# Performance work log

Measured on AMD Instinct MI355X. Metric: run time of the kernel, lower is better.

## Reference

```python
import jax, jax.numpy as jnp
import numpy as np

NUM_HEADS = 8
D_MODEL = 256
DIM = D_MODEL // NUM_HEADS  # 32
EPS = 1e-6


def _proj(x, W, b):
    # Conv1d with kernel_size=1 == channel-mixing matmul over length axis
    return jnp.einsum('oi,bil->bol', W, x) + b[None, :, None]


def _linear_attention(q, k, v):
    # q,k,v: [B, dim, heads, L]
    q = jax.nn.elu(q) + 1.0
    k = jax.nn.elu(k) + 1.0
    L = v.shape[3]
    v = v / L
    # KV: [B, dim_v, dim_k, heads]
    KV = jnp.einsum('bdhm,bqhm->bqdh', k, v)
    # Z: [B, heads, L]
    Z = 1.0 / (jnp.einsum('bdhm,bdh->bhm', q, k.sum(3)) + EPS)
    # out: [B, dim, heads, L]
    return jnp.einsum('bdhm,bqdh,bhm->bqhm', q, KV, Z) * L


def setup_inputs() -> dict:
    key = jax.random.key(0)
    ks = jax.random.split(key, 11)
    B, L = 8, 4096
    s = 0.05
    return {
        'query': jax.random.normal(ks[0], (B, D_MODEL, L), dtype=jnp.float32),
        'key':   jax.random.normal(ks[1], (B, D_MODEL, L), dtype=jnp.float32),
        'value': jax.random.normal(ks[2], (B, D_MODEL, L), dtype=jnp.float32),
        'Wq': jax.random.normal(ks[3], (D_MODEL, D_MODEL), dtype=jnp.float32) * s,
        'bq': jnp.zeros((D_MODEL,), dtype=jnp.float32),
        'Wk': jax.random.normal(ks[4], (D_MODEL, D_MODEL), dtype=jnp.float32) * s,
        'bk': jnp.zeros((D_MODEL,), dtype=jnp.float32),
        'Wv': jax.random.normal(ks[5], (D_MODEL, D_MODEL), dtype=jnp.float32) * s,
        'bv': jnp.zeros((D_MODEL,), dtype=jnp.float32),
        'Wm': jax.random.normal(ks[6], (D_MODEL, D_MODEL), dtype=jnp.float32) * s,
        'bm': jnp.zeros((D_MODEL,), dtype=jnp.float32),
    }


def reference(query, key, value, Wq, bq, Wk, bk, Wv, bv, Wm, bm):
    B = query.shape[0]
    q = _proj(query, Wq, bq).reshape(B, DIM, NUM_HEADS, -1)
    k = _proj(key,   Wk, bk).reshape(B, DIM, NUM_HEADS, -1)
    v = _proj(value, Wv, bv).reshape(B, DIM, NUM_HEADS, -1)
    x = _linear_attention(q, k, v)           # [B, dim, heads, L]
    x = x.reshape(B, D_MODEL, -1)            # merge heads back to channels
    return jnp.einsum('oi,bil->bol', Wm, x) + bm[None, :, None]
```

## Files before the change

kernel.cpp:

```cpp
#include <hip/hip_runtime.h>
#include <math.h>

#define D_MODEL 256
#define NHEADS 8
#define HDIM 32
#define BATCH 8
#define SEQL 4096
#define EPS 1e-6f

typedef _Float16 f16;
typedef _Float16 f16x4 __attribute__((ext_vector_type(4)));
typedef _Float16 f16x8 __attribute__((ext_vector_type(8)));
typedef float f32x4 __attribute__((ext_vector_type(4)));

__device__ __forceinline__ float elu1(float x) {
    return x > 0.f ? x + 1.f : __expf(x);
}

__global__ void prep_kernel(const float* __restrict__ Wq, const float* __restrict__ Wk,
                            const float* __restrict__ Wv, const float* __restrict__ Wm,
                            const float* __restrict__ bq, const float* __restrict__ bk,
                            const float* __restrict__ bv,
                            f16* __restrict__ w16, float* __restrict__ bperm,
                            float* __restrict__ KVz) {
    const int bid = blockIdx.x;
    if (bid < 1024) {
        int idx = bid * 256 + threadIdx.x;
        int mat = idx >> 16, r = (idx >> 8) & 255, c = idx & 255;
        const float* W = (mat == 0) ? Wq : (mat == 1) ? Wk : (mat == 2) ? Wv : Wm;
        float v;
        if (mat < 3) v = W[(size_t)(((r & 31) << 3) + (r >> 5)) * 256 + c];
        else         v = W[(size_t)r * 256 + (((c & 31) << 3) + (c >> 5))];
        w16[idx] = (f16)v;
    } else if (bid == 1024) {
        int t = threadIdx.x;
        bperm[0 * 256 + t] = bq[((t & 31) << 3) + (t >> 5)];
        bperm[1 * 256 + t] = bk[((t & 31) << 3) + (t >> 5)];
        bperm[2 * 256 + t] = bv[((t & 31) << 3) + (t >> 5)];
    } else {
        int i = (bid - 1025) * 256 + threadIdx.x;
        KVz[i] = 0.f;
    }
}

#define BSTR 40
__global__ __launch_bounds__(256, 3) void gemm_stage1(
    const float* __restrict__ Xq, const float* __restrict__ Xk, const float* __restrict__ Xv,
    const f16* __restrict__ w16, const float* __restrict__ bperm,
    f16* __restrict__ yq, f16* __restrict__ yk, f16* __restrict__ yv) {
    __shared__ __align__(16) char smem[18432];
    f16* Bs = (f16*)smem;
    f16* Cb = (f16*)smem;

    const int z = blockIdx.z;
    const int which = z >> 3;
    const int b = z & 7;
    const float* X = (which == 0) ? Xq : (which == 1) ? Xk : Xv;
    const f16* W = w16 + which * 65536;
    f16* Y = (which == 0) ? yq : (which == 1) ? yk : yv;
    const float* bp = bperm + which * 256;

    const int l0 = blockIdx.x * 128;
    const int m0 = blockIdx.y * 128;
    const int tid = threadIdx.x;
    const int wave = tid >> 6, lane = tid & 63;
    const int wm = wave >> 1, wn = wave & 1;
    const int ln = lane & 15, quad = lane >> 4;
    const int bp8 = tid & 7;
    const int bg = tid >> 3;

    const float* Xbase = X + ((size_t)b * D_MODEL + 4 * bp8) * SEQL + l0 + 4 * bg;
    const f16* Wb[4];
#pragma unroll
    for (int mf = 0; mf < 4; ++mf)
        Wb[mf] = W + (size_t)(m0 + wm * 64 + mf * 16 + ln) * 256 + quad * 8;

    float4 xr[4];
    f16x8 afc[4], afn[4];

#define LOADX(K0) do { \
        const float* xb_ = Xbase + (size_t)(K0) * SEQL; \
        xr[0] = *(const float4*)(xb_ + 0 * SEQL); \
        xr[1] = *(const float4*)(xb_ + 1 * SEQL); \
        xr[2] = *(const float4*)(xb_ + 2 * SEQL); \
        xr[3] = *(const float4*)(xb_ + 3 * SEQL); \
    } while (0)

#define STOREB() do { \
        f16x4 w_; \
        w_[0] = (f16)xr[0].x; w_[1] = (f16)xr[1].x; w_[2] = (f16)xr[2].x; w_[3] = (f16)xr[3].x; \
        *(f16x4*)&Bs[(4 * bg + 0) * BSTR + 4 * bp8] = w_; \
        w_[0] = (f16)xr[0].y; w_[1] = (f16)xr[1].y; w_[2] = (f16)xr[2].y; w_[3] = (f16)xr[3].y; \
        *(f16x4*)&Bs[(4 * bg + 1) * BSTR + 4 * bp8] = w_; \
        w_[0] = (f16)xr[0].z; w_[1] = (f16)xr[1].z; w_[2] = (f16)xr[2].z; w_[3] = (f16)xr[3].z; \
        *(f16x4*)&Bs[(4 * bg + 2) * BSTR + 4 * bp8] = w_; \
        w_[0] = (f16)xr[0].w; w_[1] = (f16)xr[1].w; w_[2] = (f16)xr[2].w; w_[3] = (f16)xr[3].w; \
        *(f16x4*)&Bs[(4 * bg + 3) * BSTR + 4 * bp8] = w_; \
    } while (0)

    f32x4 acc[4][4];
#pragma unroll
    for (int mf = 0; mf < 4; ++mf)
#pragma unroll
        for (int nf = 0; nf < 4; ++nf)
#pragma unroll
            for (int r = 0; r < 4; ++r) acc[mf][nf][r] = 0.f;

    LOADX(0);
#pragma unroll
    for (int mf = 0; mf < 4; ++mf) afc[mf] = *(const f16x8*)(Wb[mf] + 0);

#pragma unroll
    for (int it = 0; it < 8; ++it) {
        const int k0 = it * 32;
        __syncthreads();
        STOREB();
        __syncthreads();
        if (it < 7) {
            LOADX(k0 + 32);
#pragma unroll
            for (int mf = 0; mf < 4; ++mf)
                afn[mf] = *(const f16x8*)(Wb[mf] + k0 + 32);
        }
        f16x8 bf[4];
#pragma unroll
        for (int nf = 0; nf < 4; ++nf)
            bf[nf] = *(const f16x8*)&Bs[(wn * 64 + nf * 16 + ln) * BSTR + quad * 8];
#pragma unroll
        for (int mf = 0; mf < 4; ++mf)
#pragma unroll
            for (int nf = 0; nf < 4; ++nf)
                acc[mf][nf] = __builtin_amdgcn_mfma_f32_16x16x32_f16(afc[mf], bf[nf], acc[mf][nf], 0, 0, 0);
#pragma unroll
        for (int mf = 0; mf < 4; ++mf) afc[mf] = afn[mf];
    }

    float bv_[4][4];
#pragma unroll
    for (int mf = 0; mf < 4; ++mf)
#pragma unroll
        for (int r = 0; r < 4; ++r)
            bv_[mf][r] = bp[m0 + wm * 64 + mf * 16 + quad * 4 + r];
#pragma unroll
    for (int pass = 0; pass < 2; ++pass) {
        __syncthreads();
        if (wm == pass) {
#pragma unroll
            for (int mf = 0; mf < 4; ++mf)
#pragma unroll
                for (int nf = 0; nf < 4; ++nf) {
                    const int olocal = mf * 16 + quad * 4;
                    const int llocal = wn * 64 + nf * 16 + ln;
                    f16x4 w;
#pragma unroll
                    for (int r = 0; r < 4; ++r) w[r] = (f16)(acc[mf][nf][r] + bv_[mf][r]);
                    *(f16x4*)&Cb[llocal * 72 + olocal] = w;
                }
        }
        __syncthreads();
        const int l = tid >> 1, half = tid & 1;
        f16* yr = Y + ((size_t)(b * SEQL + l0 + l)) * 256 + m0 + pass * 64 + half * 32;
#pragma unroll
        for (int u = 0; u < 4; ++u)
            *(f16x8*)(yr + u * 8) = *(const f16x8*)&Cb[l * 72 + half * 32 + u * 8];
    }
}

__global__ __launch_bounds__(256) void kv_kernel(
    const f16* __restrict__ kp, const f16* __restrict__ vp,
    float* __restrict__ KV, float* __restrict__ ksum) {
    const int bh = blockIdx.y;
    const int b = bh >> 3, h = bh & 7;
    const int lbase = blockIdx.x * (SEQL / 16);
    __shared__ float ks[64][33];
    __shared__ float vs[64][33];
    const int t = threadIdx.x;
    const int lrow = t >> 2, seg = t & 3;
    const int kd = t & 31, qg = t >> 5;
    float a0 = 0.f, a1 = 0.f, a2 = 0.f, a3 = 0.f, ss = 0.f;
    for (int lc = 0; lc < SEQL / 16; lc += 64) {
        __syncthreads();
        const size_t off = ((size_t)(b * SEQL + lbase + lc + lrow)) * 256 + h * 32 + seg * 8;
        f16x8 k8 = *(const f16x8*)(kp + off);
        f16x8 v8 = *(const f16x8*)(vp + off);
#pragma unroll
        for (int j = 0; j < 8; ++j) {
            ks[lrow][seg * 8 + j] = elu1((float)k8[j]);
            vs[lrow][seg * 8 + j] = (float)v8[j];
        }
        __syncthreads();
#pragma unroll 8
        for (int li = 0; li < 64; ++li) {
            const float kk = ks[li][kd];
            ss += kk;
            a0 += kk * vs[li][qg * 4 + 0];
            a1 += kk * vs[li][qg * 4 + 1];
            a2 += kk * vs[li][qg * 4 + 2];
            a3 += kk * vs[li][qg * 4 + 3];
        }
    }
    float* KVb = KV + (size_t)(b * NHEADS + h) * HDIM * HDIM;
    atomicAdd(&KVb[(qg * 4 + 0) * HDIM + kd], a0);
    atomicAdd(&KVb[(qg * 4 + 1) * HDIM + kd], a1);
    atomicAdd(&KVb[(qg * 4 + 2) * HDIM + kd], a2);
    atomicAdd(&KVb[(qg * 4 + 3) * HDIM + kd], a3);
    if (qg == 0) atomicAdd(&ksum[(size_t)(b * NHEADS + h) * HDIM + kd], ss);
}

__global__ __launch_bounds__(256) void attn_out_kernel(
    const f16* __restrict__ qp, const float* __restrict__ KV,
    const float* __restrict__ ksum, const f16* __restrict__ wm16,
    const float* __restrict__ bm, float* __restrict__ out) {
    __shared__ __align__(16) f16 xs[64 * 264];
    __shared__ __align__(16) f16 Baug[8 * 48 * 40];
    __shared__ float dens[8][64];
    const int b = blockIdx.y;
    const int l0 = blockIdx.x * 64;
    const int t = threadIdx.x;
    const int wave = t >> 6, lane = t & 63;
    const int ln = lane & 15, quad = lane >> 4;

    {
        const int h = t >> 5, qd = t & 31;
        const float* kvp = KV + ((size_t)(b * NHEADS + h) * HDIM + qd) * HDIM;
        f16* dst = &Baug[(h * 48 + qd) * 40];
#pragma unroll
        for (int i = 0; i < 32; i += 4) {
            float4 a = *(const float4*)(kvp + i);
            f16x4 w4;
            w4[0] = (f16)a.x; w4[1] = (f16)a.y; w4[2] = (f16)a.z; w4[3] = (f16)a.w;
            *(f16x4*)(dst + i) = w4;
        }
        Baug[(h * 48 + 32) * 40 + qd] = (f16)ksum[(size_t)(b * NHEADS + h) * HDIM + qd];
    }
    {
        const int row = t & 63, cg = t >> 6;
        const f16* qr = qp + ((size_t)(b * SEQL + l0 + row)) * 256 + cg * 64;
        f16* dst = &xs[row * 264 + cg * 64];
#pragma unroll
        for (int u = 0; u < 64; u += 8) {
            f16x8 v = *(const f16x8*)(qr + u);
            f16x8 w;
#pragma unroll
            for (int j = 0; j < 8; ++j) w[j] = (f16)elu1((float)v[j]);
            *(f16x8*)(dst + u) = w;
        }
    }
    __syncthreads();
#pragma unroll
    for (int hh = 0; hh < 2; ++hh) {
        const int h = wave * 2 + hh;
        f16x8 a_s[4], b_s[3];
#pragma unroll
        for (int mf = 0; mf < 4; ++mf)
            a_s[mf] = *(const f16x8*)&xs[(mf * 16 + ln) * 264 + h * 32 + quad * 8];
#pragma unroll
        for (int nf = 0; nf < 3; ++nf)
            b_s[nf] = *(const f16x8*)&Baug[(h * 48 + nf * 16 + ln) * 40 + quad * 8];
        f32x4 C[4][3];
#pragma unroll
        for (int mf = 0; mf < 4; ++mf)
#pragma unroll
            for (int nf = 0; nf < 3; ++nf) {
#pragma unroll
                for (int r = 0; r < 4; ++r) C[mf][nf][r] = 0.f;
                C[mf][nf] = __builtin_amdgcn_mfma_f32_16x16x32_f16(a_s[mf], b_s[nf], C[mf][nf], 0, 0, 0);
            }
        if (ln == 0) {
#pragma unroll
            for (int mf = 0; mf < 4; ++mf)
#pragma unroll
                for (int r = 0; r < 4; ++r)
                    dens[h][mf * 16 + quad * 4 + r] = C[mf][2][r];
        }
        __syncthreads();
#pragma unroll
        for (int mf = 0; mf < 4; ++mf)
#pragma unroll
            for (int r = 0; r < 4; ++r) {
                const int l = mf * 16 + quad * 4 + r;
                const float rd = __builtin_amdgcn_rcpf(dens[h][l] + EPS);
#pragma unroll
                for (int nf = 0; nf < 2; ++nf)
                    xs[l * 264 + h * 32 + nf * 16 + ln] = (f16)(C[mf][nf][r] * rd);
            }
        __syncthreads();
    }
    f32x4 acc[4][4];
#pragma unroll
    for (int mf = 0; mf < 4; ++mf)
#pragma unroll
        for (int nf = 0; nf < 4; ++nf)
#pragma unroll
            for (int r = 0; r < 4; ++r) acc[mf][nf][r] = 0.f;
    const f16* Wb[4];
#pragma unroll
    for (int mf = 0; mf < 4; ++mf)
        Wb[mf] = wm16 + (size_t)(wave * 64 + mf * 16 + ln) * 256 + quad * 8;
    f16x8 afc[4], afn[4];
#pragma unroll
    for (int mf = 0; mf < 4; ++mf) afc[mf] = *(const f16x8*)(Wb[mf] + 0);
#pragma unroll
    for (int it = 0; it < 8; ++it) {
        const int k0 = it * 32;
        if (it < 7) {
#pragma unroll
            for (int mf = 0; mf < 4; ++mf) afn[mf] = *(const f16x8*)(Wb[mf] + k0 + 32);
        }
        f16x8 bf[4];
#pragma unroll
        for (int nf = 0; nf < 4; ++nf)
            bf[nf] = *(const f16x8*)&xs[(nf * 16 + ln) * 264 + k0 + quad * 8];
#pragma unroll
        for (int mf = 0; mf < 4; ++mf)
#pragma unroll
            for (int nf = 0; nf < 4; ++nf)
                acc[mf][nf] = __builtin_amdgcn_mfma_f32_16x16x32_f16(afc[mf], bf[nf], acc[mf][nf], 0, 0, 0);
#pragma unroll
        for (int mf = 0; mf < 4; ++mf) afc[mf] = afn[mf];
    }
#pragma unroll
    for (int mf = 0; mf < 4; ++mf) {
        const int o = wave * 64 + mf * 16 + quad * 4;
#pragma unroll
        for (int r = 0; r < 4; ++r) {
            const float bb = bm[o + r];
            float* op = out + ((size_t)(b * D_MODEL + o + r)) * SEQL + l0;
#pragma unroll
            for (int nf = 0; nf < 4; ++nf)
                op[nf * 16 + ln] = acc[mf][nf][r] + bb;
        }
    }
}

extern "C" void kernel_launch(void* const* d_in, const int* in_sizes, int n_in,
                              void* d_out, int out_size, void* d_ws, size_t ws_size,
                              hipStream_t stream) {
    const float* query = (const float*)d_in[0];
    const float* key_  = (const float*)d_in[1];
    const float* value = (const float*)d_in[2];
    const float* Wq = (const float*)d_in[3];
    const float* bq = (const float*)d_in[4];
    const float* Wk = (const float*)d_in[5];
    const float* bk = (const float*)d_in[6];
    const float* Wv = (const float*)d_in[7];
    const float* bv = (const float*)d_in[8];
    const float* Wm = (const float*)d_in[9];
    const float* bm = (const float*)d_in[10];

    char* w = (char*)d_ws;
    f16*   w16   = (f16*)w;
    float* bperm = (float*)(w + 524288);
    float* KV    = (float*)(w + 528384);
    float* ksum  = (float*)(w + 790528);
    f16*   qp    = (f16*)(w + 802816);
    f16*   kp    = qp + (size_t)BATCH * SEQL * 256;
    f16*   vp    = kp + (size_t)BATCH * SEQL * 256;

    prep_kernel<<<1289, 256, 0, stream>>>(Wq, Wk, Wv, Wm, bq, bk, bv, w16, bperm, KV);

    gemm_stage1<<<dim3(SEQL / 128, 2, 24), 256, 0, stream>>>(
        query, key_, value, w16, bperm, qp, kp, vp);

    kv_kernel<<<dim3(16, BATCH * NHEADS), 256, 0, stream>>>(kp, vp, KV, ksum);

    attn_out_kernel<<<dim3(SEQL / 64, BATCH), 256, 0, stream>>>(
        qp, KV, ksum, w16 + 3 * 65536, bm, (float*)d_out);
}
```

Measured before the change: 223.0 us.

## Fuse K/V projections with KV reduction in one projection kernel

The projection GEMM now handles K, V and Q for one tile in a single block and runs them back to back. The ELU-transformed K tile and the V tile stay in shared memory, and the per-tile KV outer product and key sum are computed with MFMA and atomically added to global memory. This removes the fp16 K/V round trip through global memory and the separate kv_kernel launch. The B buffer is also double-buffered so one sync per iteration suffices. In exchange the grid shrinks to one third of its blocks, shared memory rises to 52KB, which may limit occupancy, and there are more atomics.

```diff
diff --git a/kernel.cpp b/kernel.cpp
--- a/kernel.cpp
+++ b/kernel.cpp
@@ -44,58 +44,58 @@
 }
 
 #define BSTR 40
-__global__ __launch_bounds__(256, 3) void gemm_stage1(
+__global__ __launch_bounds__(256, 3) void gemm_fused(
     const float* __restrict__ Xq, const float* __restrict__ Xk, const float* __restrict__ Xv,
     const f16* __restrict__ w16, const float* __restrict__ bperm,
-    f16* __restrict__ yq, f16* __restrict__ yk, f16* __restrict__ yv) {
-    __shared__ __align__(16) char smem[18432];
-    f16* Bs = (f16*)smem;
-    f16* Cb = (f16*)smem;
-
-    const int z = blockIdx.z;
-    const int which = z >> 3;
-    const int b = z & 7;
-    const float* X = (which == 0) ? Xq : (which == 1) ? Xk : Xv;
-    const f16* W = w16 + which * 65536;
-    f16* Y = (which == 0) ? yq : (which == 1) ? yk : yv;
-    const float* bp = bperm + which * 256;
-
+    f16* __restrict__ qp, float* __restrict__ KV, float* __restrict__ ksum) {
+    __shared__ __align__(16) char smem[53248];
+    f16* kT = (f16*)smem;
+    f16* B0 = (f16*)(smem + 32768);
+    f16* B1 = (f16*)(smem + 43008);
+    f16* vT = (f16*)(smem + 32768);
+    f16* Cb = (f16*)(smem + 32768);
+
+    const int b = blockIdx.z;
     const int l0 = blockIdx.x * 128;
     const int m0 = blockIdx.y * 128;
     const int tid = threadIdx.x;
     const int wave = tid >> 6, lane = tid & 63;
     const int wm = wave >> 1, wn = wave & 1;
     const int ln = lane & 15, quad = lane >> 4;
-    const int bp8 = tid & 7;
-    const int bg = tid >> 3;
-
-    const float* Xbase = X + ((size_t)b * D_MODEL + 4 * bp8) * SEQL + l0 + 4 * bg;
-    const f16* Wb[4];
+    const int g = tid >> 5;
+    const int bg = tid & 31;
+
+    const float* Xarr[3] = {Xk, Xv, Xq};
+    const int woff[3] = {65536, 131072, 0};
+    const int boff[3] = {256, 512, 0};
+    const size_t xoff = ((size_t)(b * D_MODEL) + 4 * g) * SEQL + l0 + 4 * bg;
+
+    int wrow[4];
 #pragma unroll
     for (int mf = 0; mf < 4; ++mf)
-        Wb[mf] = W + (size_t)(m0 + wm * 64 + mf * 16 + ln) * 256 + quad * 8;
+        wrow[mf] = (m0 + wm * 64 + mf * 16 + ln) * 256 + quad * 8;
 
     float4 xr[4];
     f16x8 afc[4], afn[4];
 
-#define LOADX(K0) do { \
-        const float* xb_ = Xbase + (size_t)(K0) * SEQL; \
+#define LOADX(PH, K0) do { \
+        const float* xb_ = Xarr[PH] + xoff + (size_t)(K0) * SEQL; \
         xr[0] = *(const float4*)(xb_ + 0 * SEQL); \
         xr[1] = *(const float4*)(xb_ + 1 * SEQL); \
         xr[2] = *(const float4*)(xb_ + 2 * SEQL); \
         xr[3] = *(const float4*)(xb_ + 3 * SEQL); \
     } while (0)
 
-#define STOREB() do { \
+#define STOREB(BUF) do { \
         f16x4 w_; \
         w_[0] = (f16)xr[0].x; w_[1] = (f16)xr[1].x; w_[2] = (f16)xr[2].x; w_[3] = (f16)xr[3].x; \
-        *(f16x4*)&Bs[(4 * bg + 0) * BSTR + 4 * bp8] = w_; \
+        *(f16x4*)&BUF[(4 * bg + 0) * BSTR + 4 * g] = w_; \
         w_[0] = (f16)xr[0].y; w_[1] = (f16)xr[1].y; w_[2] = (f16)xr[2].y; w_[3] = (f16)xr[3].y; \
-        *(f16x4*)&Bs[(4 * bg + 1) * BSTR + 4 * bp8] = w_; \
+        *(f16x4*)&BUF[(4 * bg + 1) * BSTR + 4 * g] = w_; \
         w_[0] = (f16)xr[0].z; w_[1] = (f16)xr[1].z; w_[2] = (f16)xr[2].z; w_[3] = (f16)xr[3].z; \
-        *(f16x4*)&Bs[(4 * bg + 2) * BSTR + 4 * bp8] = w_; \
+        *(f16x4*)&BUF[(4 * bg + 2) * BSTR + 4 * g] = w_; \
         w_[0] = (f16)xr[0].w; w_[1] = (f16)xr[1].w; w_[2] = (f16)xr[2].w; w_[3] = (f16)xr[3].w; \
-        *(f16x4*)&Bs[(4 * bg + 3) * BSTR + 4 * bp8] = w_; \
+        *(f16x4*)&BUF[(4 * bg + 3) * BSTR + 4 * g] = w_; \
     } while (0)
 
     f32x4 acc[4][4];
@@ -106,105 +106,186 @@
 #pragma unroll
             for (int r = 0; r < 4; ++r) acc[mf][nf][r] = 0.f;
 
-    LOADX(0);
-#pragma unroll
-    for (int mf = 0; mf < 4; ++mf) afc[mf] = *(const f16x8*)(Wb[mf] + 0);
-
-#pragma unroll
-    for (int it = 0; it < 8; ++it) {
-        const int k0 = it * 32;
+    LOADX(0, 0);
+#pragma unroll
+    for (int mf = 0; mf < 4; ++mf) afc[mf] = *(const f16x8*)(w16 + woff[0] + wrow[mf]);
+
+#pragma unroll
+    for (int it = 0; it < 24; ++it) {
+        const int k0 = (it & 7) * 32;
+        f16* buf = (it & 1) ? B1 : B0;
+        STOREB(buf);
         __syncthreads();
-        STOREB();
-        __syncthreads();
-        if (it < 7) {
-            LOADX(k0 + 32);
-#pragma unroll
-            for (int mf = 0; mf < 4; ++mf)
-                afn[mf] = *(const f16x8*)(Wb[mf] + k0 + 32);
+        if (it < 23) {
+            const int phn = (it + 1) >> 3, k0n = ((it + 1) & 7) * 32;
+            LOADX(phn, k0n);
+#pragma unroll
+            for (int mf = 0; mf < 4; ++mf)
+                afn[mf] = *(const f16x8*)(w16 + woff[phn] + wrow[mf] + k0n);
         }
         f16x8 bf[4];
 #pragma unroll
         for (int nf = 0; nf < 4; ++nf)
-            bf[nf] = *(const f16x8*)&Bs[(wn * 64 + nf * 16 + ln) * BSTR + quad * 8];
+            bf[nf] = *(const f16x8*)&buf[(wn * 64 + nf * 16 + ln) * BSTR + quad * 8];
 #pragma unroll
         for (int mf = 0; mf < 4; ++mf)
 #pragma unroll
             for (int nf = 0; nf < 4; ++nf)
                 acc[mf][nf] = __builtin_amdgcn_mfma_f32_16x16x32_f16(afc[mf], bf[nf], acc[mf][nf], 0, 0, 0);
-#pragma unroll
-        for (int mf = 0; mf < 4; ++mf) afc[mf] = afn[mf];
-    }
-
-    float bv_[4][4];
-#pragma unroll
-    for (int mf = 0; mf < 4; ++mf)
-#pragma unroll
-        for (int r = 0; r < 4; ++r)
-            bv_[mf][r] = bp[m0 + wm * 64 + mf * 16 + quad * 4 + r];
-#pragma unroll
-    for (int pass = 0; pass < 2; ++pass) {
-        __syncthreads();
-        if (wm == pass) {
-#pragma unroll
-            for (int mf = 0; mf < 4; ++mf)
-#pragma unroll
-                for (int nf = 0; nf < 4; ++nf) {
-                    const int olocal = mf * 16 + quad * 4;
-                    const int llocal = wn * 64 + nf * 16 + ln;
-                    f16x4 w;
-#pragma unroll
-                    for (int r = 0; r < 4; ++r) w[r] = (f16)(acc[mf][nf][r] + bv_[mf][r]);
-                    *(f16x4*)&Cb[llocal * 72 + olocal] = w;
+        if (it < 23) {
+#pragma unroll
+            for (int mf = 0; mf < 4; ++mf) afc[mf] = afn[mf];
+        }
+
+        if (it == 7) {
+            const float* bpk = bperm + boff[0] + m0 + wm * 64;
+            float sp[4][4];
+#pragma unroll
+            for (int mf = 0; mf < 4; ++mf)
+#pragma unroll
+                for (int r = 0; r < 4; ++r) {
+                    const float bb = bpk[mf * 16 + quad * 4 + r];
+                    const int o = wm * 64 + mf * 16 + quad * 4 + r;
+                    float s = 0.f;
+#pragma unroll
+                    for (int nf = 0; nf < 4; ++nf) {
+                        const int l = wn * 64 + nf * 16 + ln;
+                        const float e = elu1(acc[mf][nf][r] + bb);
+                        s += e;
+                        *(f16*)((char*)kT + ((o * 256 + l * 2) ^ ((o & 7) << 4))) = (f16)e;
+                    }
+                    sp[mf][r] = s;
                 }
-        }
-        __syncthreads();
-        const int l = tid >> 1, half = tid & 1;
-        f16* yr = Y + ((size_t)(b * SEQL + l0 + l)) * 256 + m0 + pass * 64 + half * 32;
-#pragma unroll
-        for (int u = 0; u < 4; ++u)
-            *(f16x8*)(yr + u * 8) = *(const f16x8*)&Cb[l * 72 + half * 32 + u * 8];
-    }
-}
-
-__global__ __launch_bounds__(256) void kv_kernel(
-    const f16* __restrict__ kp, const f16* __restrict__ vp,
-    float* __restrict__ KV, float* __restrict__ ksum) {
-    const int bh = blockIdx.y;
-    const int b = bh >> 3, h = bh & 7;
-    const int lbase = blockIdx.x * (SEQL / 16);
-    __shared__ float ks[64][33];
-    __shared__ float vs[64][33];
-    const int t = threadIdx.x;
-    const int lrow = t >> 2, seg = t & 3;
-    const int kd = t & 31, qg = t >> 5;
-    float a0 = 0.f, a1 = 0.f, a2 = 0.f, a3 = 0.f, ss = 0.f;
-    for (int lc = 0; lc < SEQL / 16; lc += 64) {
-        __syncthreads();
-        const size_t off = ((size_t)(b * SEQL + lbase + lc + lrow)) * 256 + h * 32 + seg * 8;
-        f16x8 k8 = *(const f16x8*)(kp + off);
-        f16x8 v8 = *(const f16x8*)(vp + off);
-#pragma unroll
-        for (int j = 0; j < 8; ++j) {
-            ks[lrow][seg * 8 + j] = elu1((float)k8[j]);
-            vs[lrow][seg * 8 + j] = (float)v8[j];
-        }
-        __syncthreads();
-#pragma unroll 8
-        for (int li = 0; li < 64; ++li) {
-            const float kk = ks[li][kd];
-            ss += kk;
-            a0 += kk * vs[li][qg * 4 + 0];
-            a1 += kk * vs[li][qg * 4 + 1];
-            a2 += kk * vs[li][qg * 4 + 2];
-            a3 += kk * vs[li][qg * 4 + 3];
-        }
-    }
-    float* KVb = KV + (size_t)(b * NHEADS + h) * HDIM * HDIM;
-    atomicAdd(&KVb[(qg * 4 + 0) * HDIM + kd], a0);
-    atomicAdd(&KVb[(qg * 4 + 1) * HDIM + kd], a1);
-    atomicAdd(&KVb[(qg * 4 + 2) * HDIM + kd], a2);
-    atomicAdd(&KVb[(qg * 4 + 3) * HDIM + kd], a3);
-    if (qg == 0) atomicAdd(&ksum[(size_t)(b * NHEADS + h) * HDIM + kd], ss);
+#pragma unroll
+            for (int st = 1; st < 16; st <<= 1)
+#pragma unroll
+                for (int mf = 0; mf < 4; ++mf)
+#pragma unroll
+                    for (int r = 0; r < 4; ++r)
+                        sp[mf][r] += __shfl_xor(sp[mf][r], st);
+            if (ln == 0) {
+                float* kss = ksum + (size_t)b * 256 + m0 + wm * 64;
+#pragma unroll
+                for (int mf = 0; mf < 4; ++mf)
+#pragma unroll
+                    for (int r = 0; r < 4; ++r)
+                        atomicAdd(&kss[mf * 16 + quad * 4 + r], sp[mf][r]);
+            }
+#pragma unroll
+            for (int mf = 0; mf < 4; ++mf)
+#pragma unroll
+                for (int nf = 0; nf < 4; ++nf)
+#pragma unroll
+                    for (int r = 0; r < 4; ++r) acc[mf][nf][r] = 0.f;
+        }
+
+        if (it == 15) {
+            const float* bpv = bperm + boff[1] + m0 + wm * 64;
+#pragma unroll
+            for (int mf = 0; mf < 4; ++mf)
+#pragma unroll
+                for (int r = 0; r < 4; ++r) {
+                    const float bb = bpv[mf * 16 + quad * 4 + r];
+#pragma unroll
+                    for (int nf = 0; nf < 4; ++nf) acc[mf][nf][r] += bb;
+                }
+            f32x4 kvacc[2][2];
+#pragma unroll
+            for (int ti = 0; ti < 2; ++ti)
+#pragma unroll
+                for (int tj = 0; tj < 2; ++tj)
+#pragma unroll
+                    for (int r = 0; r < 4; ++r) kvacc[ti][tj][r] = 0.f;
+            const int hloc = wave;
+#pragma unroll
+            for (int pass = 0; pass < 2; ++pass) {
+                __syncthreads();
+                if (wn == pass) {
+#pragma unroll
+                    for (int mf = 0; mf < 4; ++mf)
+#pragma unroll
+                        for (int nf = 0; nf < 4; ++nf)
+#pragma unroll
+                            for (int r = 0; r < 4; ++r) {
+                                const int o = wm * 64 + mf * 16 + quad * 4 + r;
+                                const int l = nf * 16 + ln;
+                                *(f16*)((char*)vT + ((o * 128 + l * 2) ^ ((o & 7) << 4))) = (f16)acc[mf][nf][r];
+                            }
+                }
+                __syncthreads();
+#pragma unroll
+                for (int ks = 0; ks < 2; ++ks) {
+                    f16x8 av[2], bv2[2];
+#pragma unroll
+                    for (int t2 = 0; t2 < 2; ++t2) {
+                        const int row = hloc * 32 + t2 * 16 + ln;
+                        av[t2]  = *(const f16x8*)((char*)kT +
+                                    ((row * 256 + (pass * 64 + ks * 32 + quad * 8) * 2) ^ ((row & 7) << 4)));
+                        bv2[t2] = *(const f16x8*)((char*)vT +
+                                    ((row * 128 + (ks * 32 + quad * 8) * 2) ^ ((row & 7) << 4)));
+                    }
+#pragma unroll
+                    for (int ti = 0; ti < 2; ++ti)
+#pragma unroll
+                        for (int tj = 0; tj < 2; ++tj)
+                            kvacc[ti][tj] = __builtin_amdgcn_mfma_f32_16x16x32_f16(av[ti], bv2[tj], kvacc[ti][tj], 0, 0, 0);
+                }
+            }
+            __syncthreads();
+            float* KVb = KV + ((size_t)(b * NHEADS) + (m0 >> 5) + hloc) * 1024;
+#pragma unroll
+            for (int ti = 0; ti < 2; ++ti)
+#pragma unroll
+                for (int tj = 0; tj < 2; ++tj)
+#pragma unroll
+                    for (int r = 0; r < 4; ++r) {
+                        const int kd = ti * 16 + quad * 4 + r;
+                        const int qd = tj * 16 + ln;
+                        atomicAdd(&KVb[qd * 32 + kd], kvacc[ti][tj][r]);
+                    }
+#pragma unroll
+            for (int mf = 0; mf < 4; ++mf)
+#pragma unroll
+                for (int nf = 0; nf < 4; ++nf)
+#pragma unroll
+                    for (int r = 0; r < 4; ++r) acc[mf][nf][r] = 0.f;
+        }
+
+        if (it == 23) {
+            const float* bpq = bperm + boff[2] + m0 + wm * 64;
+            float bv_[4][4];
+#pragma unroll
+            for (int mf = 0; mf < 4; ++mf)
+#pragma unroll
+                for (int r = 0; r < 4; ++r)
+                    bv_[mf][r] = bpq[mf * 16 + quad * 4 + r];
+#pragma unroll
+            for (int pass = 0; pass < 2; ++pass) {
+                __syncthreads();
+                if (wm == pass) {
+#pragma unroll
+                    for (int mf = 0; mf < 4; ++mf)
+#pragma unroll
+                        for (int nf = 0; nf < 4; ++nf) {
+                            const int olocal = mf * 16 + quad * 4;
+                            const int llocal = wn * 64 + nf * 16 + ln;
+                            f16x4 w;
+#pragma unroll
+                            for (int r = 0; r < 4; ++r) w[r] = (f16)(acc[mf][nf][r] + bv_[mf][r]);
+                            *(f16x4*)&Cb[llocal * 72 + olocal] = w;
+                        }
+                }
+                __syncthreads();
+                const int l = tid >> 1, half = tid & 1;
+                f16* yr = qp + ((size_t)(b * SEQL + l0 + l)) * 256 + m0 + pass * 64 + half * 32;
+#pragma unroll
+                for (int u = 0; u < 4; ++u)
+                    *(f16x8*)(yr + u * 8) = *(const f16x8*)&Cb[l * 72 + half * 32 + u * 8];
+            }
+        }
+    }
+#undef LOADX
+#undef STOREB
 }
 
 __global__ __launch_bounds__(256) void attn_out_kernel(
@@ -354,15 +435,11 @@
     float* KV    = (float*)(w + 528384);
     float* ksum  = (float*)(w + 790528);
     f16*   qp    = (f16*)(w + 802816);
-    f16*   kp    = qp + (size_t)BATCH * SEQL * 256;
-    f16*   vp    = kp + (size_t)BATCH * SEQL * 256;
 
     prep_kernel<<<1289, 256, 0, stream>>>(Wq, Wk, Wv, Wm, bq, bk, bv, w16, bperm, KV);
 
-    gemm_stage1<<<dim3(SEQL / 128, 2, 24), 256, 0, stream>>>(
-        query, key_, value, w16, bperm, qp, kp, vp);
-
-    kv_kernel<<<dim3(16, BATCH * NHEADS), 256, 0, stream>>>(kp, vp, KV, ksum);
+    gemm_fused<<<dim3(SEQL / 128, 2, BATCH), 256, 0, stream>>>(
+        query, key_, value, w16, bperm, qp, KV, ksum);
 
     attn_out_kernel<<<dim3(SEQL / 64, BATCH), 256, 0, stream>>>(
         qp, KV, ksum, w16 + 3 * 65536, bm, (float*)d_out);
```

Measured after the change: 410.3 us. +84.0%, slower.
